# Kernel tuning notes

Measured on AMD Instinct MI355X. Metric: run time of the kernel, lower is better.

Reference implementation:

```python
import jax, jax.numpy as jnp
import numpy as np

E, TOPK = 32, 2            # hardcoded in LossMOEDecoder
D, HID, BOT, OUT = 768, 2048, 256, 768
B, S = 2, 128


def setup_inputs() -> dict:
    key = jax.random.key(0)
    ks = jax.random.split(key, 7)
    p = lambda k, shape: jax.random.normal(k, shape, dtype=jnp.float32) * 0.02
    return {
        "x": jax.random.normal(ks[0], (B, S, D), dtype=jnp.float32),
        "gate_w": p(ks[1], (E, D)),                 # MoEGate.weight
        "W1": p(ks[2], (E, D, HID)),  "b1": jnp.zeros((E, HID), jnp.float32),
        "W2": p(ks[3], (E, HID, HID)), "b2": jnp.zeros((E, HID), jnp.float32),
        "W3": p(ks[4], (E, HID, BOT)), "b3": jnp.zeros((E, BOT), jnp.float32),
        "Wl": p(ks[5], (E, BOT, OUT)), "bl": jnp.zeros((E, OUT), jnp.float32),
    }


def reference(x, gate_w, W1, b1, W2, b2, W3, b3, Wl, bl):
    Bz, Sl, d = x.shape
    xt = x.reshape(-1, d)                                    # [N, d] tokens
    # --- gate: softmax then top-k (values permutation-invariant vs torch sorted=False)
    scores = jax.nn.softmax(xt @ gate_w.T, axis=-1)          # [N, E]
    topk_w, topk_idx = jax.lax.top_k(scores, TOPK)           # [N, k]
    topk_w = topk_w / (topk_w.sum(-1, keepdims=True) + 1e-20)  # norm_topk_prob
    # --- experts: batched over the (small, fixed) expert axis; exact GELU as nn.GELU
    gelu = lambda v: jax.nn.gelu(v, approximate=False)
    h = gelu(jnp.einsum('nd,edh->enh', xt, W1) + b1[:, None, :])   # [E, N, HID]
    h = gelu(jnp.einsum('enh,ehg->eng', h, W2) + b2[:, None, :])   # [E, N, HID]
    z = jnp.einsum('eng,egb->enb', h, W3) + b3[:, None, :]         # [E, N, BOT]
    out_all = jnp.einsum('enb,ebo->eno', z, Wl) + bl[:, None, :]   # [E, N, OUT]
    # --- combine: gather each token's top-k expert outputs, weighted sum
    sel = jnp.take_along_axis(out_all.transpose(1, 0, 2),          # [N, E, OUT]
                              topk_idx[:, :, None], axis=1)        # [N, k, OUT]
    y = (sel * topk_w[:, :, None]).sum(axis=1)                     # [N, OUT]
    return y.reshape(Bz, Sl, OUT)
```

## Files before the change

kernel.cpp:

```cpp
#include <hip/hip_runtime.h>
#include <math.h>

#define NEXP 32
#define NTOK 256
#define DIMD 768
#define DHID 2048
#define DBOT 256
#define DOUT 768
#define NSLOT 512
#define CHUNK 16

__global__ __launch_bounds__(64) void gate_kernel(
    const float* __restrict__ x, const float* __restrict__ gw,
    const float* __restrict__ bl, float* __restrict__ y,
    int* __restrict__ topk_idx, float* __restrict__ topk_w,
    float* __restrict__ z, float* __restrict__ A) {
  const int n = blockIdx.x;
  const int l = threadIdx.x;
  {
    const float4 zv = {0.f, 0.f, 0.f, 0.f};
    float4* zp = (float4*)(z + n * 512 + l * 8);
    zp[0] = zv; zp[1] = zv;
    float4* ap = (float4*)(A + (size_t)n * 4096 + l * 64);
#pragma unroll
    for (int j = 0; j < 16; j++) ap[j] = zv;
  }
  const float* xr = x + n * DIMD;
  float xs[12];
#pragma unroll
  for (int j = 0; j < 12; j++) xs[j] = xr[l + 64 * j];
  float logit[NEXP];
#pragma unroll
  for (int e = 0; e < NEXP; e++) {
    const float* g = gw + e * DIMD;
    float p = 0.f;
#pragma unroll
    for (int j = 0; j < 12; j++) p = fmaf(xs[j], g[l + 64 * j], p);
#pragma unroll
    for (int m = 1; m < 64; m <<= 1) p += __shfl_xor(p, m);
    logit[e] = p;
  }
  int i0 = 0; float m0 = logit[0];
#pragma unroll
  for (int e = 1; e < NEXP; e++) { if (logit[e] > m0) { m0 = logit[e]; i0 = e; } }
  int i1 = -1; float m1 = -3.4e38f;
#pragma unroll
  for (int e = 0; e < NEXP; e++) { if (e != i0 && logit[e] > m1) { m1 = logit[e]; i1 = e; } }
  const float e1 = expf(m1 - m0);
  const float w0 = 1.f / (1.f + e1);
  const float w1 = e1 * w0;
  if (l == 0) {
    topk_idx[2 * n] = i0; topk_idx[2 * n + 1] = i1;
    topk_w[2 * n] = w0;  topk_w[2 * n + 1] = w1;
  }
  const float* bl0 = bl + i0 * DOUT;
  const float* bl1 = bl + i1 * DOUT;
#pragma unroll
  for (int j = 0; j < 12; j++) {
    const int o = l + 64 * j;
    y[n * DOUT + o] = fmaf(w0, bl0[o], w1 * bl1[o]);
  }
}

__global__ __launch_bounds__(256) void build_lists(
    const int* __restrict__ topk_idx, const float* __restrict__ topk_w,
    int* __restrict__ counts, int* __restrict__ offsets,
    int* __restrict__ tok_list, float* __restrict__ tok_wt,
    int* __restrict__ slot_expert) {
  __shared__ int cnt[NEXP], base[NEXP], fill[NEXP];
  const int t = threadIdx.x;
  if (t < NEXP) { cnt[t] = 0; fill[t] = 0; }
  __syncthreads();
  const int e0 = topk_idx[2 * t], e1 = topk_idx[2 * t + 1];
  atomicAdd(&cnt[e0], 1);
  atomicAdd(&cnt[e1], 1);
  __syncthreads();
  if (t == 0) { int s = 0; for (int i = 0; i < NEXP; i++) { base[i] = s; s += cnt[i]; } }
  __syncthreads();
  const int p0 = atomicAdd(&fill[e0], 1);
  tok_list[base[e0] + p0] = t; tok_wt[base[e0] + p0] = topk_w[2 * t];
  slot_expert[base[e0] + p0] = e0;
  const int p1 = atomicAdd(&fill[e1], 1);
  tok_list[base[e1] + p1] = t; tok_wt[base[e1] + p1] = topk_w[2 * t + 1];
  slot_expert[base[e1] + p1] = e1;
  if (t < NEXP) { counts[t] = cnt[t]; offsets[t] = base[t]; }
}

__device__ __forceinline__ float gelu_f(float v) {
  return 0.5f * v * (1.f + erff(v * 0.70710678118654752f));
}

__global__ __launch_bounds__(256) void gelu_pass(
    const float* __restrict__ A, const float* __restrict__ bias,
    float* __restrict__ Bout, float* __restrict__ Azero,
    const int* __restrict__ slot_expert) {
  const int slot = blockIdx.x;
  const int e = slot_expert[slot];
  const int c0 = threadIdx.x * 8;
  const float* ap = A + (size_t)slot * DHID + c0;
  const float* bp = bias + (size_t)e * DHID + c0;
  float* op = Bout + (size_t)slot * DHID + c0;
  float* zp = Azero + (size_t)slot * DHID + c0;
  const float4 zz = {0.f, 0.f, 0.f, 0.f};
#pragma unroll
  for (int j = 0; j < 8; j += 4) {
    const float4 a = *(const float4*)(ap + j);
    const float4 b = *(const float4*)(bp + j);
    float4 o;
    o.x = gelu_f(a.x + b.x); o.y = gelu_f(a.y + b.y);
    o.z = gelu_f(a.z + b.z); o.w = gelu_f(a.w + b.w);
    *(float4*)(op + j) = o;
    *(float4*)(zp + j) = zz;
  }
}

template <int MODE>
__global__ __launch_bounds__(256) void ff_kernel(
    const float* __restrict__ Ain, const float* __restrict__ W,
    const float* __restrict__ Bias, float* __restrict__ Out,
    const int* __restrict__ offsets, const int* __restrict__ counts,
    const int* __restrict__ tok_list, const float* __restrict__ tok_wt,
    int KTOT, int NCT, int INS, int coltiles) {
  __shared__ float act[CHUNK * 256];
  const int tid  = threadIdx.x;
  const int lane = tid & 63;
  const int wave = tid >> 6;
  const int cg   = wave & 1;
  const int kh   = wave >> 1;
  const int e    = blockIdx.y;
  const int ct   = blockIdx.x % coltiles;
  const int kb   = blockIdx.x / coltiles;
  const int cnt  = counts[e];
  const int off  = offsets[e];
  const int cb   = ct * 256;
  const int wcol2 = cg * 128 + 2 * lane;
  const float* Wblk = W + ((size_t)e * KTOT + (size_t)kb * 256 + kh * 128) * NCT + cb + wcol2;

  for (int tc0 = 0; tc0 < cnt; tc0 += CHUNK) {
    const int tcn = min(CHUNK, cnt - tc0);
    if (MODE == 3) {
      const int t  = tid >> 4;
      const int r0 = (tid & 15) * 16;
      const int slot = min(off + tc0 + t, NSLOT - 1);
      const float* src  = Ain + (size_t)slot * INS + r0;
      const float* bsrc = Bias + (size_t)e * KTOT + r0;
      float* dst = act + t * 256 + r0;
#pragma unroll
      for (int j = 0; j < 16; j += 4) {
        float4 v = *(const float4*)(src + j);
        const float4 bv = *(const float4*)(bsrc + j);
        v.x += bv.x; v.y += bv.y; v.z += bv.z; v.w += bv.w;
        *(float4*)(dst + j) = v;
      }
    } else {
#pragma unroll
      for (int i = 0; i < 4; i++) {
        const int t = wave * 4 + i;
        const int slot = min(off + tc0 + t, NSLOT - 1);
        const int row  = (MODE == 0) ? tok_list[slot] : slot;
        const float* src = Ain + (size_t)row * INS + (size_t)kb * 256 + lane * 4;
        __builtin_amdgcn_global_load_lds(
            (const __attribute__((address_space(1))) void*)src,
            (__attribute__((address_space(3))) void*)(act + t * 256),
            16, 0, 0);
      }
    }
    __syncthreads();

    float acc0[CHUNK], acc1[CHUNK];
#pragma unroll
    for (int t = 0; t < CHUNK; t++) { acc0[t] = 0.f; acc1[t] = 0.f; }
    float2 wbuf[4][4];
#pragma unroll
    for (int j = 0; j < 4; j++) {
      wbuf[0][j] = *(const float2*)(Wblk + (size_t)j * NCT);
      wbuf[1][j] = *(const float2*)(Wblk + (size_t)(4 + j) * NCT);
    }
#pragma unroll 4
    for (int g = 0; g < 32; ++g) {
      const int cur = g & 3;
      const int nxt = (g + 2) & 3;
      const int gp  = min(g + 2, 31);
      const float* wn = Wblk + (size_t)(4 * gp) * NCT;
#pragma unroll
      for (int j = 0; j < 4; j++) wbuf[nxt][j] = *(const float2*)(wn + (size_t)j * NCT);
      const float* bp = act + kh * 128 + 4 * g;
#pragma unroll
      for (int t = 0; t < CHUNK; t++) {
        const float4 xv = *(const float4*)(bp + t * 256);
        acc0[t] = fmaf(xv.x, wbuf[cur][0].x, acc0[t]);
        acc1[t] = fmaf(xv.x, wbuf[cur][0].y, acc1[t]);
        acc0[t] = fmaf(xv.y, wbuf[cur][1].x, acc0[t]);
        acc1[t] = fmaf(xv.y, wbuf[cur][1].y, acc1[t]);
        acc0[t] = fmaf(xv.z, wbuf[cur][2].x, acc0[t]);
        acc1[t] = fmaf(xv.z, wbuf[cur][2].y, acc1[t]);
        acc0[t] = fmaf(xv.w, wbuf[cur][3].x, acc0[t]);
        acc1[t] = fmaf(xv.w, wbuf[cur][3].y, acc1[t]);
      }
    }

    __syncthreads();
    if (kh == 1) {
#pragma unroll
      for (int t = 0; t < CHUNK; t++) {
        act[t * 256 + wcol2]     = acc0[t];
        act[t * 256 + wcol2 + 1] = acc1[t];
      }
    }
    __syncthreads();
    if (kh == 0) {
      for (int t = 0; t < tcn; t++) {
        const float s0 = acc0[t] + act[t * 256 + wcol2];
        const float s1 = acc1[t] + act[t * 256 + wcol2 + 1];
        const int slot = off + tc0 + t;
        if (MODE <= 2) {
          atomicAdd(&Out[(size_t)slot * NCT + cb + wcol2], s0);
          atomicAdd(&Out[(size_t)slot * NCT + cb + wcol2 + 1], s1);
        } else {
          const int trow = tok_list[slot];
          const float wgt = tok_wt[slot];
          atomicAdd(&Out[(size_t)trow * NCT + cb + wcol2], wgt * s0);
          atomicAdd(&Out[(size_t)trow * NCT + cb + wcol2 + 1], wgt * s1);
        }
      }
    }
    __syncthreads();
  }
}

extern "C" void kernel_launch(void* const* d_in, const int* in_sizes, int n_in,
                              void* d_out, int out_size, void* d_ws, size_t ws_size,
                              hipStream_t stream) {
  const float* x  = (const float*)d_in[0];
  const float* gw = (const float*)d_in[1];
  const float* W1 = (const float*)d_in[2];
  const float* b1 = (const float*)d_in[3];
  const float* W2 = (const float*)d_in[4];
  const float* b2 = (const float*)d_in[5];
  const float* W3 = (const float*)d_in[6];
  const float* b3 = (const float*)d_in[7];
  const float* Wl = (const float*)d_in[8];
  const float* bl = (const float*)d_in[9];
  float* y  = (float*)d_out;
  float* ws = (float*)d_ws;

  float* topk_w   = ws;
  int*   topk_idx = (int*)(ws + 512);
  int*   counts   = (int*)(ws + 1024);
  int*   offsets  = (int*)(ws + 1056);
  int*   tok_list = (int*)(ws + 1088);
  float* tok_wt   = ws + 1600;
  int*   slot_exp = (int*)(ws + 2112);
  float* A = ws + 4096;
  float* B = A + (size_t)NSLOT * DHID;
  float* z = B + (size_t)NSLOT * DHID;

  gate_kernel<<<NTOK, 64, 0, stream>>>(x, gw, bl, y, topk_idx, topk_w, z, A);
  build_lists<<<1, 256, 0, stream>>>(topk_idx, topk_w, counts, offsets, tok_list, tok_wt, slot_exp);
  ff_kernel<0><<<dim3(24, 32), 256, 0, stream>>>(x, W1, nullptr, A, offsets, counts,
                                                 tok_list, tok_wt, DIMD, DHID, DIMD, 8);
  gelu_pass<<<NSLOT, 256, 0, stream>>>(A, b1, B, A, slot_exp);
  ff_kernel<1><<<dim3(64, 32), 256, 0, stream>>>(B, W2, nullptr, A, offsets, counts,
                                                 tok_list, tok_wt, DHID, DHID, DHID, 8);
  gelu_pass<<<NSLOT, 256, 0, stream>>>(A, b2, B, A, slot_exp);
  ff_kernel<2><<<dim3(8, 32), 256, 0, stream>>>(B, W3, nullptr, z, offsets, counts,
                                                tok_list, tok_wt, DHID, DBOT, DHID, 1);
  ff_kernel<3><<<dim3(3, 32), 256, 0, stream>>>(z, Wl, b3, y, offsets, counts,
                                                tok_list, tok_wt, DBOT, DOUT, DBOT, 3);
}
```

Baseline: 464.2 us.

## Restructure expert GEMMs with transposed 32-token LDS tiles and wider column blocks

```diff
diff --git a/kernel.cpp b/kernel.cpp
--- a/kernel.cpp
+++ b/kernel.cpp
@@ -8,7 +8,6 @@
 #define DBOT 256
 #define DOUT 768
 #define NSLOT 512
-#define CHUNK 16
 
 __global__ __launch_bounds__(64) void gate_kernel(
     const float* __restrict__ x, const float* __restrict__ gw,
@@ -114,117 +113,196 @@
   }
 }
 
-template <int MODE>
-__global__ __launch_bounds__(256) void ff_kernel(
-    const float* __restrict__ Ain, const float* __restrict__ W,
-    const float* __restrict__ Bias, float* __restrict__ Out,
-    const int* __restrict__ offsets, const int* __restrict__ counts,
-    const int* __restrict__ tok_list, const float* __restrict__ tok_wt,
-    int KTOT, int NCT, int INS, int coltiles) {
-  __shared__ float act[CHUNK * 256];
-  const int tid  = threadIdx.x;
-  const int lane = tid & 63;
-  const int wave = tid >> 6;
-  const int cg   = wave & 1;
-  const int kh   = wave >> 1;
-  const int e    = blockIdx.y;
-  const int ct   = blockIdx.x % coltiles;
-  const int kb   = blockIdx.x / coltiles;
-  const int cnt  = counts[e];
-  const int off  = offsets[e];
-  const int cb   = ct * 256;
-  const int wcol2 = cg * 128 + 2 * lane;
-  const float* Wblk = W + ((size_t)e * KTOT + (size_t)kb * 256 + kh * 128) * NCT + cb + wcol2;
-
-  for (int tc0 = 0; tc0 < cnt; tc0 += CHUNK) {
-    const int tcn = min(CHUNK, cnt - tc0);
-    if (MODE == 3) {
-      const int t  = tid >> 4;
-      const int r0 = (tid & 15) * 16;
-      const int slot = min(off + tc0 + t, NSLOT - 1);
-      const float* src  = Ain + (size_t)slot * INS + r0;
-      const float* bsrc = Bias + (size_t)e * KTOT + r0;
-      float* dst = act + t * 256 + r0;
+template <int KR, int GATHER>
+__device__ __forceinline__ void stage_tr(
+    float* __restrict__ act_t, const float* __restrict__ Ain, int INS,
+    const int* __restrict__ tok_list, int off, int tc0, int tcn, int kbase,
+    int tid, const float* __restrict__ bfold) {
+  const int tok = tid & 31;
+  const int kk  = tid >> 5;
+  if (kk < (KR >> 4)) {
+    float v[16];
+    if (tok < tcn) {
+      const int slot = off + tc0 + tok;
+      const int row  = GATHER ? tok_list[slot] : slot;
+      const float* src = Ain + (size_t)row * INS + kbase + kk * 16;
 #pragma unroll
       for (int j = 0; j < 16; j += 4) {
-        float4 v = *(const float4*)(src + j);
-        const float4 bv = *(const float4*)(bsrc + j);
-        v.x += bv.x; v.y += bv.y; v.z += bv.z; v.w += bv.w;
-        *(float4*)(dst + j) = v;
+        float4 q = *(const float4*)(src + j);
+        if (bfold) {
+          const float4 b = *(const float4*)(bfold + kbase + kk * 16 + j);
+          q.x += b.x; q.y += b.y; q.z += b.z; q.w += b.w;
+        }
+        v[j] = q.x; v[j + 1] = q.y; v[j + 2] = q.z; v[j + 3] = q.w;
       }
     } else {
 #pragma unroll
-      for (int i = 0; i < 4; i++) {
-        const int t = wave * 4 + i;
-        const int slot = min(off + tc0 + t, NSLOT - 1);
-        const int row  = (MODE == 0) ? tok_list[slot] : slot;
-        const float* src = Ain + (size_t)row * INS + (size_t)kb * 256 + lane * 4;
-        __builtin_amdgcn_global_load_lds(
-            (const __attribute__((address_space(1))) void*)src,
-            (__attribute__((address_space(3))) void*)(act + t * 256),
-            16, 0, 0);
+      for (int j = 0; j < 16; j++) v[j] = 0.f;
+    }
+#pragma unroll
+    for (int j = 0; j < 16; j++) act_t[(kk * 16 + j) * 32 + tok] = v[j];
+  }
+}
+
+__device__ __forceinline__ void row_fma(
+    const float* __restrict__ arow, float2 w, float* acc0, float* acc1) {
+#pragma unroll
+  for (int i = 0; i < 8; i++) {
+    const float4 xv = *(const float4*)(arow + 4 * i);
+    acc0[4 * i]     = fmaf(xv.x, w.x, acc0[4 * i]);
+    acc1[4 * i]     = fmaf(xv.x, w.y, acc1[4 * i]);
+    acc0[4 * i + 1] = fmaf(xv.y, w.x, acc0[4 * i + 1]);
+    acc1[4 * i + 1] = fmaf(xv.y, w.y, acc1[4 * i + 1]);
+    acc0[4 * i + 2] = fmaf(xv.z, w.x, acc0[4 * i + 2]);
+    acc1[4 * i + 2] = fmaf(xv.z, w.y, acc1[4 * i + 2]);
+    acc0[4 * i + 3] = fmaf(xv.w, w.x, acc0[4 * i + 3]);
+    acc1[4 * i + 3] = fmaf(xv.w, w.y, acc1[4 * i + 3]);
+  }
+}
+
+template <int MODE>
+__global__ __launch_bounds__(512, 2) void ff_lin(
+    const float* __restrict__ Ain, const float* __restrict__ W,
+    float* __restrict__ Out,
+    const int* __restrict__ offsets, const int* __restrict__ counts,
+    const int* __restrict__ tok_list,
+    int KTOT, int INS) {
+  __shared__ float act_t[256 * 32];
+  const int tid = threadIdx.x;
+  const int e   = blockIdx.y;
+  const int ct  = blockIdx.x & 1;
+  const int kb  = blockIdx.x >> 1;
+  const int cnt = counts[e];
+  const int off = offsets[e];
+  const int col = ct * 1024 + 2 * tid;
+  const float* Wcol = W + ((size_t)e * KTOT + (size_t)kb * 256) * 2048 + col;
+
+  for (int tc0 = 0; tc0 < cnt; tc0 += 32) {
+    const int tcn = min(32, cnt - tc0);
+    stage_tr<256, MODE == 0>(act_t, Ain, INS, tok_list, off, tc0, tcn,
+                             kb * 256, tid, nullptr);
+    __syncthreads();
+
+    float acc0[32], acc1[32];
+#pragma unroll
+    for (int t = 0; t < 32; t++) { acc0[t] = 0.f; acc1[t] = 0.f; }
+    float2 wbuf[4];
+    wbuf[0] = *(const float2*)(Wcol);
+    wbuf[1] = *(const float2*)(Wcol + 2048);
+#pragma unroll 4
+    for (int r = 0; r < 256; ++r) {
+      const int cur = r & 3;
+      const int nxt = (r + 2) & 3;
+      const int rp  = min(r + 2, 255);
+      wbuf[nxt] = *(const float2*)(Wcol + (size_t)rp * 2048);
+      row_fma(act_t + r * 32, wbuf[cur], acc0, acc1);
+    }
+    __syncthreads();
+
+#pragma unroll
+    for (int t = 0; t < 32; t++) {
+      if (t < tcn) {
+        const int slot = off + tc0 + t;
+        atomicAdd(&Out[(size_t)slot * 2048 + col], acc0[t]);
+        atomicAdd(&Out[(size_t)slot * 2048 + col + 1], acc1[t]);
       }
     }
-    __syncthreads();
-
-    float acc0[CHUNK], acc1[CHUNK];
-#pragma unroll
-    for (int t = 0; t < CHUNK; t++) { acc0[t] = 0.f; acc1[t] = 0.f; }
-    float2 wbuf[4][4];
-#pragma unroll
-    for (int j = 0; j < 4; j++) {
-      wbuf[0][j] = *(const float2*)(Wblk + (size_t)j * NCT);
-      wbuf[1][j] = *(const float2*)(Wblk + (size_t)(4 + j) * NCT);
-    }
+  }
+}
+
+__global__ __launch_bounds__(512, 2) void ff_bot(
+    const float* __restrict__ Ain, const float* __restrict__ W,
+    float* __restrict__ Out,
+    const int* __restrict__ offsets, const int* __restrict__ counts) {
+  __shared__ float act_t[256 * 32];
+  const int tid = threadIdx.x;
+  const int e   = blockIdx.y;
+  const int kb  = blockIdx.x;
+  const int cnt = counts[e];
+  const int off = offsets[e];
+  const int sg  = tid >> 7;
+  const int lt  = tid & 127;
+  const int col = 2 * lt;
+  const float* Wcol = W + ((size_t)e * 2048 + (size_t)kb * 256) * 256 + col;
+
+  for (int tc0 = 0; tc0 < cnt; tc0 += 32) {
+    const int tcn = min(32, cnt - tc0);
+    stage_tr<256, 0>(act_t, Ain, DHID, nullptr, off, tc0, tcn, kb * 256, tid, nullptr);
+    __syncthreads();
+
+    float acc0[32], acc1[32];
+#pragma unroll
+    for (int t = 0; t < 32; t++) { acc0[t] = 0.f; acc1[t] = 0.f; }
+    float2 wbuf[4];
+    wbuf[0] = *(const float2*)(Wcol + (size_t)sg * 256);
+    wbuf[1] = *(const float2*)(Wcol + (size_t)(sg + 4) * 256);
 #pragma unroll 4
-    for (int g = 0; g < 32; ++g) {
-      const int cur = g & 3;
-      const int nxt = (g + 2) & 3;
-      const int gp  = min(g + 2, 31);
-      const float* wn = Wblk + (size_t)(4 * gp) * NCT;
-#pragma unroll
-      for (int j = 0; j < 4; j++) wbuf[nxt][j] = *(const float2*)(wn + (size_t)j * NCT);
-      const float* bp = act + kh * 128 + 4 * g;
-#pragma unroll
-      for (int t = 0; t < CHUNK; t++) {
-        const float4 xv = *(const float4*)(bp + t * 256);
-        acc0[t] = fmaf(xv.x, wbuf[cur][0].x, acc0[t]);
-        acc1[t] = fmaf(xv.x, wbuf[cur][0].y, acc1[t]);
-        acc0[t] = fmaf(xv.y, wbuf[cur][1].x, acc0[t]);
-        acc1[t] = fmaf(xv.y, wbuf[cur][1].y, acc1[t]);
-        acc0[t] = fmaf(xv.z, wbuf[cur][2].x, acc0[t]);
-        acc1[t] = fmaf(xv.z, wbuf[cur][2].y, acc1[t]);
-        acc0[t] = fmaf(xv.w, wbuf[cur][3].x, acc0[t]);
-        acc1[t] = fmaf(xv.w, wbuf[cur][3].y, acc1[t]);
+    for (int i = 0; i < 64; ++i) {
+      const int cur = i & 3;
+      const int nxt = (i + 2) & 3;
+      const int ip  = min(i + 2, 63);
+      wbuf[nxt] = *(const float2*)(Wcol + (size_t)(sg + 4 * ip) * 256);
+      row_fma(act_t + (sg + 4 * i) * 32, wbuf[cur], acc0, acc1);
+    }
+    __syncthreads();
+
+#pragma unroll
+    for (int t = 0; t < 32; t++) {
+      if (t < tcn) {
+        const int slot = off + tc0 + t;
+        atomicAdd(&Out[(size_t)slot * DBOT + col], acc0[t]);
+        atomicAdd(&Out[(size_t)slot * DBOT + col + 1], acc1[t]);
       }
     }
-
-    __syncthreads();
-    if (kh == 1) {
-#pragma unroll
-      for (int t = 0; t < CHUNK; t++) {
-        act[t * 256 + wcol2]     = acc0[t];
-        act[t * 256 + wcol2 + 1] = acc1[t];
+  }
+}
+
+__global__ __launch_bounds__(384, 2) void ff_out(
+    const float* __restrict__ Ain, const float* __restrict__ W,
+    const float* __restrict__ b3, float* __restrict__ y,
+    const int* __restrict__ offsets, const int* __restrict__ counts,
+    const int* __restrict__ tok_list, const float* __restrict__ tok_wt) {
+  __shared__ float act_t[128 * 32];
+  const int tid = threadIdx.x;
+  const int e   = blockIdx.y;
+  const int kb  = blockIdx.x;
+  const int cnt = counts[e];
+  const int off = offsets[e];
+  const int col = 2 * tid;
+  const float* Wcol = W + ((size_t)e * DBOT + (size_t)kb * 128) * 768 + col;
+  const float* bfold = b3 + (size_t)e * DBOT;
+
+  for (int tc0 = 0; tc0 < cnt; tc0 += 32) {
+    const int tcn = min(32, cnt - tc0);
+    stage_tr<128, 0>(act_t, Ain, DBOT, nullptr, off, tc0, tcn, kb * 128, tid, bfold);
+    __syncthreads();
+
+    float acc0[32], acc1[32];
+#pragma unroll
+    for (int t = 0; t < 32; t++) { acc0[t] = 0.f; acc1[t] = 0.f; }
+    float2 wbuf[4];
+    wbuf[0] = *(const float2*)(Wcol);
+    wbuf[1] = *(const float2*)(Wcol + 768);
+#pragma unroll 4
+    for (int r = 0; r < 128; ++r) {
+      const int cur = r & 3;
+      const int nxt = (r + 2) & 3;
+      const int rp  = min(r + 2, 127);
+      wbuf[nxt] = *(const float2*)(Wcol + (size_t)rp * 768);
+      row_fma(act_t + r * 32, wbuf[cur], acc0, acc1);
+    }
+    __syncthreads();
+
+#pragma unroll
+    for (int t = 0; t < 32; t++) {
+      if (t < tcn) {
+        const int slot = off + tc0 + t;
+        const int trow = tok_list[slot];
+        const float wgt = tok_wt[slot];
+        atomicAdd(&y[(size_t)trow * DOUT + col], wgt * acc0[t]);
+        atomicAdd(&y[(size_t)trow * DOUT + col + 1], wgt * acc1[t]);
       }
     }
-    __syncthreads();
-    if (kh == 0) {
-      for (int t = 0; t < tcn; t++) {
-        const float s0 = acc0[t] + act[t * 256 + wcol2];
-        const float s1 = acc1[t] + act[t * 256 + wcol2 + 1];
-        const int slot = off + tc0 + t;
-        if (MODE <= 2) {
-          atomicAdd(&Out[(size_t)slot * NCT + cb + wcol2], s0);
-          atomicAdd(&Out[(size_t)slot * NCT + cb + wcol2 + 1], s1);
-        } else {
-          const int trow = tok_list[slot];
-          const float wgt = tok_wt[slot];
-          atomicAdd(&Out[(size_t)trow * NCT + cb + wcol2], wgt * s0);
-          atomicAdd(&Out[(size_t)trow * NCT + cb + wcol2 + 1], wgt * s1);
-        }
-      }
-    }
-    __syncthreads();
   }
 }
 
@@ -257,14 +335,12 @@
 
   gate_kernel<<<NTOK, 64, 0, stream>>>(x, gw, bl, y, topk_idx, topk_w, z, A);
   build_lists<<<1, 256, 0, stream>>>(topk_idx, topk_w, counts, offsets, tok_list, tok_wt, slot_exp);
-  ff_kernel<0><<<dim3(24, 32), 256, 0, stream>>>(x, W1, nullptr, A, offsets, counts,
-                                                 tok_list, tok_wt, DIMD, DHID, DIMD, 8);
+  ff_lin<0><<<dim3(6, 32), 512, 0, stream>>>(x, W1, A, offsets, counts, tok_list,
+                                             DIMD, DIMD);
   gelu_pass<<<NSLOT, 256, 0, stream>>>(A, b1, B, A, slot_exp);
-  ff_kernel<1><<<dim3(64, 32), 256, 0, stream>>>(B, W2, nullptr, A, offsets, counts,
-                                                 tok_list, tok_wt, DHID, DHID, DHID, 8);
+  ff_lin<1><<<dim3(16, 32), 512, 0, stream>>>(B, W2, A, offsets, counts, tok_list,
+                                              DHID, DHID);
   gelu_pass<<<NSLOT, 256, 0, stream>>>(A, b2, B, A, slot_exp);
-  ff_kernel<2><<<dim3(8, 32), 256, 0, stream>>>(B, W3, nullptr, z, offsets, counts,
-                                                tok_list, tok_wt, DHID, DBOT, DHID, 1);
-  ff_kernel<3><<<dim3(3, 32), 256, 0, stream>>>(z, Wl, b3, y, offsets, counts,
-                                                tok_list, tok_wt, DBOT, DOUT, DBOT, 3);
-}
+  ff_bot<<<dim3(8, 32), 512, 0, stream>>>(B, W3, z, offsets, counts);
+  ff_out<<<dim3(2, 32), 384, 0, stream>>>(z, Wl, b3, y, offsets, counts, tok_list, tok_wt);
+}
```

Result: faster. 452.3 us (-2.6%).

## Restructure expert FF kernel to 32-token tiles with transposed LDS activations

Applied to the files above, without the earlier changes.

```diff
diff --git a/kernel.cpp b/kernel.cpp
--- a/kernel.cpp
+++ b/kernel.cpp
@@ -8,7 +8,6 @@
 #define DBOT 256
 #define DOUT 768
 #define NSLOT 512
-#define CHUNK 16
 
 __global__ __launch_bounds__(64) void gate_kernel(
     const float* __restrict__ x, const float* __restrict__ gw,
@@ -114,117 +113,119 @@
   }
 }
 
-template <int MODE>
-__global__ __launch_bounds__(256) void ff_kernel(
+#define FMA4(A, XS, WV) \
+  A.x = fmaf(XS, WV.x, A.x); A.y = fmaf(XS, WV.y, A.y); \
+  A.z = fmaf(XS, WV.z, A.z); A.w = fmaf(XS, WV.w, A.w)
+
+template <int MODE, int CPT>
+__global__ __launch_bounds__(512, 2) void ff_kernel(
     const float* __restrict__ Ain, const float* __restrict__ W,
     const float* __restrict__ Bias, float* __restrict__ Out,
     const int* __restrict__ offsets, const int* __restrict__ counts,
     const int* __restrict__ tok_list, const float* __restrict__ tok_wt,
     int KTOT, int NCT, int INS, int coltiles) {
-  __shared__ float act[CHUNK * 256];
-  const int tid  = threadIdx.x;
-  const int lane = tid & 63;
-  const int wave = tid >> 6;
-  const int cg   = wave & 1;
-  const int kh   = wave >> 1;
-  const int e    = blockIdx.y;
-  const int ct   = blockIdx.x % coltiles;
-  const int kb   = blockIdx.x / coltiles;
-  const int cnt  = counts[e];
-  const int off  = offsets[e];
-  const int cb   = ct * 256;
-  const int wcol2 = cg * 128 + 2 * lane;
-  const float* Wblk = W + ((size_t)e * KTOT + (size_t)kb * 256 + kh * 128) * NCT + cb + wcol2;
-
-  for (int tc0 = 0; tc0 < cnt; tc0 += CHUNK) {
-    const int tcn = min(CHUNK, cnt - tc0);
-    if (MODE == 3) {
-      const int t  = tid >> 4;
-      const int r0 = (tid & 15) * 16;
-      const int slot = min(off + tc0 + t, NSLOT - 1);
-      const float* src  = Ain + (size_t)slot * INS + r0;
-      const float* bsrc = Bias + (size_t)e * KTOT + r0;
-      float* dst = act + t * 256 + r0;
-#pragma unroll
-      for (int j = 0; j < 16; j += 4) {
-        float4 v = *(const float4*)(src + j);
-        const float4 bv = *(const float4*)(bsrc + j);
-        v.x += bv.x; v.y += bv.y; v.z += bv.z; v.w += bv.w;
-        *(float4*)(dst + j) = v;
+  __shared__ float act_t[256 * 32];
+  const int tid = threadIdx.x;
+  const int tg  = tid >> 6;
+  const int cg  = tid & 63;
+  const int e   = blockIdx.y;
+  const int ct  = blockIdx.x % coltiles;
+  const int kb  = blockIdx.x / coltiles;
+  const int cnt = counts[e];
+  const int off = offsets[e];
+  const int col = ct * (64 * CPT) + cg * CPT;
+  const float* Wcol = W + ((size_t)e * KTOT + (size_t)kb * 256) * NCT + col;
+  const float* bfold = (MODE == 3) ? (Bias + (size_t)e * KTOT + kb * 256) : nullptr;
+
+  for (int tc0 = 0; tc0 < cnt; tc0 += 32) {
+    const int tcn = min(32, cnt - tc0);
+    {
+      const int tok = tid & 31;
+      const int kk  = tid >> 5;
+      float v[16];
+      if (tok < tcn) {
+        const int slot = off + tc0 + tok;
+        const int row  = (MODE == 0) ? tok_list[slot] : slot;
+        const float* src = Ain + (size_t)row * INS + kb * 256 + kk * 16;
+#pragma unroll
+        for (int j = 0; j < 16; j += 4) {
+          float4 q = *(const float4*)(src + j);
+          if (MODE == 3) {
+            const float4 b = *(const float4*)(bfold + kk * 16 + j);
+            q.x += b.x; q.y += b.y; q.z += b.z; q.w += b.w;
+          }
+          v[j] = q.x; v[j + 1] = q.y; v[j + 2] = q.z; v[j + 3] = q.w;
+        }
+      } else {
+#pragma unroll
+        for (int j = 0; j < 16; j++) v[j] = 0.f;
       }
-    } else {
-#pragma unroll
-      for (int i = 0; i < 4; i++) {
-        const int t = wave * 4 + i;
-        const int slot = min(off + tc0 + t, NSLOT - 1);
-        const int row  = (MODE == 0) ? tok_list[slot] : slot;
-        const float* src = Ain + (size_t)row * INS + (size_t)kb * 256 + lane * 4;
-        __builtin_amdgcn_global_load_lds(
-            (const __attribute__((address_space(1))) void*)src,
-            (__attribute__((address_space(3))) void*)(act + t * 256),
-            16, 0, 0);
+#pragma unroll
+      for (int j = 0; j < 16; j++) act_t[(kk * 16 + j) * 32 + tok] = v[j];
+    }
+    __syncthreads();
+
+    float4 acc0[4], acc1[4];
+#pragma unroll
+    for (int t = 0; t < 4; t++) {
+      acc0[t] = {0.f, 0.f, 0.f, 0.f};
+      acc1[t] = {0.f, 0.f, 0.f, 0.f};
+    }
+    float4 wa0[4], wa1[4];
+    wa0[0] = *(const float4*)(Wcol);
+    wa0[1] = *(const float4*)(Wcol + NCT);
+    if (CPT == 8) {
+      wa1[0] = *(const float4*)(Wcol + 4);
+      wa1[1] = *(const float4*)(Wcol + NCT + 4);
+    }
+#pragma unroll 4
+    for (int r = 0; r < 256; ++r) {
+      const int cur = r & 3;
+      const int nxt = (r + 2) & 3;
+      const int rp  = min(r + 2, 255);
+      wa0[nxt] = *(const float4*)(Wcol + (size_t)rp * NCT);
+      if (CPT == 8) wa1[nxt] = *(const float4*)(Wcol + (size_t)rp * NCT + 4);
+      const float4 xv = *(const float4*)(&act_t[r * 32 + tg * 4]);
+      FMA4(acc0[0], xv.x, wa0[cur]);
+      FMA4(acc0[1], xv.y, wa0[cur]);
+      FMA4(acc0[2], xv.z, wa0[cur]);
+      FMA4(acc0[3], xv.w, wa0[cur]);
+      if (CPT == 8) {
+        FMA4(acc1[0], xv.x, wa1[cur]);
+        FMA4(acc1[1], xv.y, wa1[cur]);
+        FMA4(acc1[2], xv.z, wa1[cur]);
+        FMA4(acc1[3], xv.w, wa1[cur]);
       }
     }
     __syncthreads();
 
-    float acc0[CHUNK], acc1[CHUNK];
-#pragma unroll
-    for (int t = 0; t < CHUNK; t++) { acc0[t] = 0.f; acc1[t] = 0.f; }
-    float2 wbuf[4][4];
-#pragma unroll
-    for (int j = 0; j < 4; j++) {
-      wbuf[0][j] = *(const float2*)(Wblk + (size_t)j * NCT);
-      wbuf[1][j] = *(const float2*)(Wblk + (size_t)(4 + j) * NCT);
-    }
-#pragma unroll 4
-    for (int g = 0; g < 32; ++g) {
-      const int cur = g & 3;
-      const int nxt = (g + 2) & 3;
-      const int gp  = min(g + 2, 31);
-      const float* wn = Wblk + (size_t)(4 * gp) * NCT;
-#pragma unroll
-      for (int j = 0; j < 4; j++) wbuf[nxt][j] = *(const float2*)(wn + (size_t)j * NCT);
-      const float* bp = act + kh * 128 + 4 * g;
-#pragma unroll
-      for (int t = 0; t < CHUNK; t++) {
-        const float4 xv = *(const float4*)(bp + t * 256);
-        acc0[t] = fmaf(xv.x, wbuf[cur][0].x, acc0[t]);
-        acc1[t] = fmaf(xv.x, wbuf[cur][0].y, acc1[t]);
-        acc0[t] = fmaf(xv.y, wbuf[cur][1].x, acc0[t]);
-        acc1[t] = fmaf(xv.y, wbuf[cur][1].y, acc1[t]);
-        acc0[t] = fmaf(xv.z, wbuf[cur][2].x, acc0[t]);
-        acc1[t] = fmaf(xv.z, wbuf[cur][2].y, acc1[t]);
-        acc0[t] = fmaf(xv.w, wbuf[cur][3].x, acc0[t]);
-        acc1[t] = fmaf(xv.w, wbuf[cur][3].y, acc1[t]);
-      }
-    }
-
-    __syncthreads();
-    if (kh == 1) {
-#pragma unroll
-      for (int t = 0; t < CHUNK; t++) {
-        act[t * 256 + wcol2]     = acc0[t];
-        act[t * 256 + wcol2 + 1] = acc1[t];
-      }
-    }
-    __syncthreads();
-    if (kh == 0) {
-      for (int t = 0; t < tcn; t++) {
-        const float s0 = acc0[t] + act[t * 256 + wcol2];
-        const float s1 = acc1[t] + act[t * 256 + wcol2 + 1];
-        const int slot = off + tc0 + t;
+#pragma unroll
+    for (int tt = 0; tt < 4; tt++) {
+      if (tg * 4 + tt < tcn) {
+        const int slot = off + tc0 + tg * 4 + tt;
         if (MODE <= 2) {
-          atomicAdd(&Out[(size_t)slot * NCT + cb + wcol2], s0);
-          atomicAdd(&Out[(size_t)slot * NCT + cb + wcol2 + 1], s1);
+          float* o = Out + (size_t)slot * NCT + col;
+          atomicAdd(o + 0, acc0[tt].x);
+          atomicAdd(o + 1, acc0[tt].y);
+          atomicAdd(o + 2, acc0[tt].z);
+          atomicAdd(o + 3, acc0[tt].w);
+          if (CPT == 8) {
+            atomicAdd(o + 4, acc1[tt].x);
+            atomicAdd(o + 5, acc1[tt].y);
+            atomicAdd(o + 6, acc1[tt].z);
+            atomicAdd(o + 7, acc1[tt].w);
+          }
         } else {
           const int trow = tok_list[slot];
           const float wgt = tok_wt[slot];
-          atomicAdd(&Out[(size_t)trow * NCT + cb + wcol2], wgt * s0);
-          atomicAdd(&Out[(size_t)trow * NCT + cb + wcol2 + 1], wgt * s1);
+          float* o = Out + (size_t)trow * DOUT + col;
+          atomicAdd(o + 0, wgt * acc0[tt].x);
+          atomicAdd(o + 1, wgt * acc0[tt].y);
+          atomicAdd(o + 2, wgt * acc0[tt].z);
+          atomicAdd(o + 3, wgt * acc0[tt].w);
         }
       }
     }
-    __syncthreads();
   }
 }
 
@@ -257,14 +258,14 @@
 
   gate_kernel<<<NTOK, 64, 0, stream>>>(x, gw, bl, y, topk_idx, topk_w, z, A);
   build_lists<<<1, 256, 0, stream>>>(topk_idx, topk_w, counts, offsets, tok_list, tok_wt, slot_exp);
-  ff_kernel<0><<<dim3(24, 32), 256, 0, stream>>>(x, W1, nullptr, A, offsets, counts,
-                                                 tok_list, tok_wt, DIMD, DHID, DIMD, 8);
+  ff_kernel<0, 8><<<dim3(12, 32), 512, 0, stream>>>(x, W1, nullptr, A, offsets, counts,
+                                                    tok_list, tok_wt, DIMD, DHID, DIMD, 4);
   gelu_pass<<<NSLOT, 256, 0, stream>>>(A, b1, B, A, slot_exp);
-  ff_kernel<1><<<dim3(64, 32), 256, 0, stream>>>(B, W2, nullptr, A, offsets, counts,
-                                                 tok_list, tok_wt, DHID, DHID, DHID, 8);
+  ff_kernel<1, 8><<<dim3(32, 32), 512, 0, stream>>>(B, W2, nullptr, A, offsets, counts,
+                                                    tok_list, tok_wt, DHID, DHID, DHID, 4);
   gelu_pass<<<NSLOT, 256, 0, stream>>>(A, b2, B, A, slot_exp);
-  ff_kernel<2><<<dim3(8, 32), 256, 0, stream>>>(B, W3, nullptr, z, offsets, counts,
-                                                tok_list, tok_wt, DHID, DBOT, DHID, 1);
-  ff_kernel<3><<<dim3(3, 32), 256, 0, stream>>>(z, Wl, b3, y, offsets, counts,
-                                                tok_list, tok_wt, DBOT, DOUT, DBOT, 3);
-}
+  ff_kernel<2, 4><<<dim3(8, 32), 512, 0, stream>>>(B, W3, nullptr, z, offsets, counts,
+                                                   tok_list, tok_wt, DHID, DBOT, DHID, 1);
+  ff_kernel<3, 4><<<dim3(3, 32), 512, 0, stream>>>(z, Wl, b3, y, offsets, counts,
+                                                   tok_list, tok_wt, DBOT, DOUT, DBOT, 3);
+}
```

Result: slower. 763.9 us (+64.6%).
